# Performance work log

Measured on AMD Instinct MI355X. Metric: run time of the kernel, lower is better.

The kernel has to match this reference:

```python
import jax, jax.numpy as jnp
import numpy as np

N_NODES = 50000


def gcn_conv(x, edge_index, edge_weight, W, b):
    """PyG GCNConv: h = x @ W.T; symmetric-norm aggregate with self loops; + bias."""
    n = x.shape[0]
    row, col = edge_index[0], edge_index[1]
    loop = jnp.arange(n)
    row_f = jnp.concatenate([row, loop])
    col_f = jnp.concatenate([col, loop])
    ew_f = jnp.concatenate([edge_weight, jnp.ones((n,), dtype=edge_weight.dtype)])
    # degree at destination (col), D^{-1/2} A D^{-1/2}
    deg = jax.ops.segment_sum(ew_f, col_f, num_segments=n)
    dinv = jnp.where(deg > 0, jax.lax.rsqrt(deg), 0.0)
    norm = dinv[row_f] * ew_f * dinv[col_f]  # [E+N]
    h = x @ W.T  # [N, out]
    msg = h[row_f] * norm[:, None]  # [E+N, out]
    out = jax.ops.segment_sum(msg, col_f, num_segments=n)
    return out + b


def prelu(x, alpha):
    return jnp.where(x >= 0, x, alpha[None, :] * x)


def setup_inputs() -> dict:
    key = jax.random.key(0)
    ks = jax.random.split(key, 8)
    in_c, hid, hid2, E = 512, 128, 64, 800000
    x = jax.random.normal(ks[0], (N_NODES, in_c), dtype=jnp.float32)
    edge_index = jax.random.randint(ks[1], (2, E), 0, N_NODES, dtype=jnp.int64)
    edge_weight = jax.random.uniform(ks[2], (E,), dtype=jnp.float32)
    s1 = 1.0 / np.sqrt(in_c)
    s2 = 1.0 / np.sqrt(hid)
    W1 = jax.random.uniform(ks[3], (hid, in_c), minval=-s1, maxval=s1, dtype=jnp.float32)
    b1 = jnp.zeros((hid,), dtype=jnp.float32)
    alpha1 = jnp.full((hid,), 0.25, dtype=jnp.float32)
    W2 = jax.random.uniform(ks[4], (hid2, hid), minval=-s2, maxval=s2, dtype=jnp.float32)
    b2 = jnp.zeros((hid2,), dtype=jnp.float32)
    alpha2 = jnp.full((hid2,), 0.25, dtype=jnp.float32)
    return {"x": x, "edge_index": edge_index, "edge_weight": edge_weight,
            "W1": W1, "b1": b1, "alpha1": alpha1,
            "W2": W2, "b2": b2, "alpha2": alpha2}


def reference(x, edge_index, edge_weight, W1, b1, alpha1, W2, b2, alpha2):
    h = gcn_conv(x, edge_index, edge_weight, W1, b1)
    h = prelu(h, alpha1)
    h = gcn_conv(h, edge_index, edge_weight, W2, b2)
    h = prelu(h, alpha2)
    return h
```

## Files before the change

kernel.cpp:

```cpp
#include <hip/hip_runtime.h>
#include <hip/hip_fp16.h>

#define IN_C 512
#define HID  128
#define HID2 64
#define CPAD 32

typedef __attribute__((ext_vector_type(8))) short short8v;
typedef __attribute__((ext_vector_type(4))) float float4v;

__device__ __forceinline__ unsigned short f2bf(float f) {
  unsigned u = __float_as_uint(f);
  unsigned r = u + 0x7FFF + ((u >> 16) & 1);
  return (unsigned short)(r >> 16);
}
__device__ __forceinline__ float bf2f(unsigned short h) {
  return __uint_as_float((unsigned)h << 16);
}
__device__ __forceinline__ uint2 pack4(unsigned short a, unsigned short b,
                                       unsigned short c, unsigned short d) {
  uint2 p;
  p.x = (unsigned)a | ((unsigned)b << 16);
  p.y = (unsigned)c | ((unsigned)d << 16);
  return p;
}
__device__ __forceinline__ void split4(float4 v, uint2& hi, uint2& lo) {
  unsigned short h0 = f2bf(v.x), h1 = f2bf(v.y), h2 = f2bf(v.z), h3 = f2bf(v.w);
  unsigned short l0 = f2bf(v.x - bf2f(h0)), l1 = f2bf(v.y - bf2f(h1));
  unsigned short l2 = f2bf(v.z - bf2f(h2)), l3 = f2bf(v.w - bf2f(h3));
  hi = pack4(h0, h1, h2, h3);
  lo = pack4(l0, l1, l2, l3);
}

__global__ void k_detect(const unsigned* __restrict__ ei, int* __restrict__ flag) {
  __shared__ int nz;
  if (threadIdx.x == 0) nz = 0;
  __syncthreads();
  if (ei[2 * threadIdx.x + 1] != 0u) atomicOr(&nz, 1);
  __syncthreads();
  if (threadIdx.x == 0) *flag = (nz == 0) ? 1 : 0;
}

__device__ __forceinline__ int edge_at(const unsigned* __restrict__ ei, int f, int i) {
  return (int)(f ? ei[2 * (size_t)i] : ei[i]);
}

__global__ void k_wsplit(const float* __restrict__ W1, const float* __restrict__ W2,
                         short* __restrict__ w1h, short* __restrict__ w1l,
                         short* __restrict__ w2h, short* __restrict__ w2l) {
  int tid = blockIdx.x * blockDim.x + threadIdx.x;
  if (tid < 128 * (IN_C / 4)) {
    int n = tid >> 7, k = (tid & 127) * 4;
    float4 v = *(const float4*)(W1 + (size_t)n * IN_C + k);
    uint2 hi, lo;
    split4(v, hi, lo);
    size_t base = (((size_t)(k >> 3)) * 128 + n) * 8 + (k & 7);
    *(uint2*)(w1h + base) = hi;
    *(uint2*)(w1l + base) = lo;
  } else if (tid < 128 * (IN_C / 4) + 64 * (HID / 4)) {
    int t = tid - 128 * (IN_C / 4);
    int n = t >> 5, k = (t & 31) * 4;
    float4 v = *(const float4*)(W2 + (size_t)n * HID + k);
    uint2 hi, lo;
    split4(v, hi, lo);
    size_t base = (((size_t)(k >> 3)) * 64 + n) * 8 + (k & 7);
    *(uint2*)(w2h + base) = hi;
    *(uint2*)(w2l + base) = lo;
  }
}

__global__ void k_cnt(const unsigned* __restrict__ ei, const int* __restrict__ flag,
                      int* __restrict__ cntp, int* __restrict__ rank, int E) {
  int f = *flag;
  int stride = gridDim.x * blockDim.x * 2;
  for (int e = (blockIdx.x * blockDim.x + threadIdx.x) * 2; e < E; e += stride) {
    int c0, c1 = -1;
    if (f) {
      if (e + 1 < E) {
        uint4 v = *(const uint4*)(ei + 2 * (size_t)(E + e));
        c0 = (int)v.x;
        c1 = (int)v.z;
      } else {
        c0 = (int)ei[2 * (size_t)(E + e)];
      }
    } else {
      if (e + 1 < E) {
        uint2 v = *(const uint2*)(ei + (size_t)E + e);
        c0 = (int)v.x;
        c1 = (int)v.y;
      } else {
        c0 = (int)ei[(size_t)E + e];
      }
    }
    rank[e] = atomicAdd(&cntp[c0 * CPAD], 1);
    if (c1 >= 0) rank[e + 1] = atomicAdd(&cntp[c1 * CPAD], 1);
  }
}

__global__ __launch_bounds__(256) void k_scanA(const int* __restrict__ cntp,
                                               int* __restrict__ part,
                                               int* __restrict__ bsum, int N) {
  __shared__ int tmp[256];
  int t = threadIdx.x;
  int idx = blockIdx.x * 1024 + t * 4;
  int4 v;
  v.x = idx + 0 < N ? cntp[(size_t)(idx + 0) * CPAD] : 0;
  v.y = idx + 1 < N ? cntp[(size_t)(idx + 1) * CPAD] : 0;
  v.z = idx + 2 < N ? cntp[(size_t)(idx + 2) * CPAD] : 0;
  v.w = idx + 3 < N ? cntp[(size_t)(idx + 3) * CPAD] : 0;
  int s = v.x + v.y + v.z + v.w;
  tmp[t] = s;
  __syncthreads();
#pragma unroll
  for (int d = 1; d < 256; d <<= 1) {
    int u = (t >= d) ? tmp[t - d] : 0;
    __syncthreads();
    tmp[t] += u;
    __syncthreads();
  }
  int excl = tmp[t] - s;
  int4 o;
  o.x = excl;
  o.y = excl + v.x;
  o.z = excl + v.x + v.y;
  o.w = excl + v.x + v.y + v.z;
  if (idx + 3 < N) {
    *(int4*)(part + idx) = o;
  } else {
    if (idx + 0 < N) part[idx + 0] = o.x;
    if (idx + 1 < N) part[idx + 1] = o.y;
    if (idx + 2 < N) part[idx + 2] = o.z;
    if (idx + 3 < N) part[idx + 3] = o.w;
  }
  if (t == 255) bsum[blockIdx.x] = tmp[255];
}

__global__ __launch_bounds__(256) void k_scanB(int* __restrict__ bsum, int nb) {
  __shared__ int tmp[256];
  int t = threadIdx.x;
  int s = (t < nb) ? bsum[t] : 0;
  tmp[t] = s;
  __syncthreads();
#pragma unroll
  for (int d = 1; d < 256; d <<= 1) {
    int u = (t >= d) ? tmp[t - d] : 0;
    __syncthreads();
    tmp[t] += u;
    __syncthreads();
  }
  bsum[t] = tmp[t] - s;
}

__global__ void k_scanC(const int* __restrict__ part, const int* __restrict__ bsum,
                        int* __restrict__ rowptr, int N, int E) {
  int i = blockIdx.x * blockDim.x + threadIdx.x;
  if (i < N) rowptr[i] = part[i] + bsum[i >> 10];
  if (i == 0) rowptr[N] = E;
}

__global__ void k_fill(const unsigned* __restrict__ ei, const int* __restrict__ flag,
                       const float* __restrict__ ew, const int* __restrict__ rowptr,
                       const int* __restrict__ rank, uint2* __restrict__ ep, int E) {
  int f = *flag;
  int stride = gridDim.x * blockDim.x;
  for (int e = blockIdx.x * blockDim.x + threadIdx.x; e < E; e += stride) {
    int r = edge_at(ei, f, e);
    int c = edge_at(ei, f, E + e);
    int p = rowptr[c] + rank[e];
    uint2 m;
    m.x = (unsigned)r;
    m.y = __float_as_uint(ew[e]);
    ep[p] = m;
  }
}

__global__ void k_degsum(const uint2* __restrict__ ep, const int* __restrict__ rowptr,
                         float* __restrict__ dinv, int N) {
  int g = blockIdx.x * blockDim.x + threadIdx.x;
  int node = g >> 4, l = g & 15;
  if (node >= N) return;
  int s = rowptr[node], epd = rowptr[node + 1];
  float sum = 0.f;
  for (int p = s + l; p < epd; p += 16) sum += __uint_as_float(ep[p].y);
  sum += __shfl_xor(sum, 1);
  sum += __shfl_xor(sum, 2);
  sum += __shfl_xor(sum, 4);
  sum += __shfl_xor(sum, 8);
  if (l == 0) {
    float d = sum + 1.0f;
    float y = rsqrtf(d);
    y = y * (1.5f - 0.5f * d * y * y);
    dinv[node] = y;
  }
}

__global__ void k_scale(uint2* __restrict__ ep, const int* __restrict__ rowptr,
                        const float* __restrict__ dinv, int N) {
  int g = blockIdx.x * blockDim.x + threadIdx.x;
  int node = g >> 4, l = g & 15;
  if (node >= N) return;
  float dn = dinv[node];
  int s = rowptr[node], epd = rowptr[node + 1];
  for (int p = s + l; p < epd; p += 16) {
    uint2 m = ep[p];
    ep[p].y = __float_as_uint(dinv[m.x] * __uint_as_float(m.y) * dn);
  }
}

__global__ __launch_bounds__(256) void k_gemm1m(const float* __restrict__ x,
                                                const short* __restrict__ w1h,
                                                const short* __restrict__ w1l,
                                                __half* __restrict__ h, int M) {
  __shared__ short xh[4][128][8], xl[4][128][8];
  __shared__ short wh[4][128][8], wl[4][128][8];
  const int t = threadIdx.x;
  const int lane = t & 63, w = t >> 6;
  const int wm = (w >> 1) * 64, wn = (w & 1) * 64;
  const int kb = lane >> 4, r16 = lane & 15;
  const int m0 = blockIdx.x * 128;

  float4v acc[4][4];
#pragma unroll
  for (int mi = 0; mi < 4; mi++)
#pragma unroll
    for (int nj = 0; nj < 4; nj++) acc[mi][nj] = (float4v)0.f;

  for (int k0 = 0; k0 < IN_C; k0 += 32) {
#pragma unroll
    for (int i = 0; i < 4; i++) {
      int idx = t + i * 256;
      int row = idx >> 3, kc = idx & 7;
      int gr = m0 + row;
      if (gr >= M) gr = M - 1;
      float4 v = *(const float4*)(x + (size_t)gr * IN_C + k0 + kc * 4);
      uint2 hi, lo;
      split4(v, hi, lo);
      int kbw = kc >> 1, s = kc & 1;
      *(uint2*)&xh[kbw][row][s * 4] = hi;
      *(uint2*)&xl[kbw][row][s * 4] = lo;
    }
#pragma unroll
    for (int i = 0; i < 2; i++) {
      int idx = t + i * 256;
      int kb2 = idx >> 7, n = idx & 127;
      size_t gbase = (((size_t)(k0 >> 3) + kb2) * 128 + n) * 8;
      *(short8v*)&wh[kb2][n][0] = *(const short8v*)(w1h + gbase);
      *(short8v*)&wl[kb2][n][0] = *(const short8v*)(w1l + gbase);
    }
    __syncthreads();

    short8v ah[4], al[4], bh[4], bl[4];
#pragma unroll
    for (int mi = 0; mi < 4; mi++) {
      ah[mi] = *(short8v*)&xh[kb][wm + mi * 16 + r16][0];
      al[mi] = *(short8v*)&xl[kb][wm + mi * 16 + r16][0];
    }
#pragma unroll
    for (int nj = 0; nj < 4; nj++) {
      bh[nj] = *(short8v*)&wh[kb][wn + nj * 16 + r16][0];
      bl[nj] = *(short8v*)&wl[kb][wn + nj * 16 + r16][0];
    }
#pragma unroll
    for (int mi = 0; mi < 4; mi++)
#pragma unroll
      for (int nj = 0; nj < 4; nj++) {
        acc[mi][nj] = __builtin_amdgcn_mfma_f32_16x16x32_bf16(ah[mi], bh[nj], acc[mi][nj], 0, 0, 0);
        acc[mi][nj] = __builtin_amdgcn_mfma_f32_16x16x32_bf16(ah[mi], bl[nj], acc[mi][nj], 0, 0, 0);
        acc[mi][nj] = __builtin_amdgcn_mfma_f32_16x16x32_bf16(al[mi], bh[nj], acc[mi][nj], 0, 0, 0);
      }
    __syncthreads();
  }

#pragma unroll
  for (int mi = 0; mi < 4; mi++)
#pragma unroll
    for (int nj = 0; nj < 4; nj++) {
#pragma unroll
      for (int b = 0; b < 4; b++) {
        int grow = m0 + wm + mi * 16 + (lane >> 4) * 4 + b;
        int gcol = wn + nj * 16 + r16;
        if (grow < M) h[(size_t)grow * HID + gcol] = __float2half(acc[mi][nj][b]);
      }
    }
}

__global__ __launch_bounds__(256) void k_gemm2m(const float* __restrict__ z,
                                                const short* __restrict__ w2h,
                                                const short* __restrict__ w2l,
                                                __half* __restrict__ h, int M) {
  __shared__ short zh[4][128][8], zl[4][128][8];
  __shared__ short wh[4][64][8], wl[4][64][8];
  const int t = threadIdx.x;
  const int lane = t & 63, w = t >> 6;
  const int wm = (w >> 1) * 64, wn = (w & 1) * 32;
  const int kb = lane >> 4, r16 = lane & 15;
  const int m0 = blockIdx.x * 128;

  float4v acc[4][2];
#pragma unroll
  for (int mi = 0; mi < 4; mi++)
#pragma unroll
    for (int nj = 0; nj < 2; nj++) acc[mi][nj] = (float4v)0.f;

  for (int k0 = 0; k0 < HID; k0 += 32) {
#pragma unroll
    for (int i = 0; i < 4; i++) {
      int idx = t + i * 256;
      int row = idx >> 3, kc = idx & 7;
      int gr = m0 + row;
      if (gr >= M) gr = M - 1;
      float4 v = *(const float4*)(z + (size_t)gr * HID + k0 + kc * 4);
      uint2 hi, lo;
      split4(v, hi, lo);
      int kbw = kc >> 1, s = kc & 1;
      *(uint2*)&zh[kbw][row][s * 4] = hi;
      *(uint2*)&zl[kbw][row][s * 4] = lo;
    }
    {
      int kb2 = t >> 6, n = t & 63;
      size_t gbase = (((size_t)(k0 >> 3) + kb2) * 64 + n) * 8;
      *(short8v*)&wh[kb2][n][0] = *(const short8v*)(w2h + gbase);
      *(short8v*)&wl[kb2][n][0] = *(const short8v*)(w2l + gbase);
    }
    __syncthreads();

    short8v ah[4], al[4], bh[2], bl[2];
#pragma unroll
    for (int mi = 0; mi < 4; mi++) {
      ah[mi] = *(short8v*)&zh[kb][wm + mi * 16 + r16][0];
      al[mi] = *(short8v*)&zl[kb][wm + mi * 16 + r16][0];
    }
#pragma unroll
    for (int nj = 0; nj < 2; nj++) {
      bh[nj] = *(short8v*)&wh[kb][wn + nj * 16 + r16][0];
      bl[nj] = *(short8v*)&wl[kb][wn + nj * 16 + r16][0];
    }
#pragma unroll
    for (int mi = 0; mi < 4; mi++)
#pragma unroll
      for (int nj = 0; nj < 2; nj++) {
        acc[mi][nj] = __builtin_amdgcn_mfma_f32_16x16x32_bf16(ah[mi], bh[nj], acc[mi][nj], 0, 0, 0);
        acc[mi][nj] = __builtin_amdgcn_mfma_f32_16x16x32_bf16(ah[mi], bl[nj], acc[mi][nj], 0, 0, 0);
        acc[mi][nj] = __builtin_amdgcn_mfma_f32_16x16x32_bf16(al[mi], bh[nj], acc[mi][nj], 0, 0, 0);
      }
    __syncthreads();
  }

#pragma unroll
  for (int mi = 0; mi < 4; mi++)
#pragma unroll
    for (int nj = 0; nj < 2; nj++) {
#pragma unroll
      for (int b = 0; b < 4; b++) {
        int grow = m0 + wm + mi * 16 + (lane >> 4) * 4 + b;
        int gcol = wn + nj * 16 + r16;
        if (grow < M) h[(size_t)grow * HID2 + gcol] = __float2half(acc[mi][nj][b]);
      }
    }
}

__global__ void k_agg1(const __half* __restrict__ h, const int* __restrict__ rowptr,
                       const uint2* __restrict__ ep, const float* __restrict__ dinv,
                       const float* __restrict__ bias, const float* __restrict__ alpha,
                       float* __restrict__ z, int N) {
  int node = blockIdx.x * 4 + (threadIdx.x >> 6);
  int lane = threadIdx.x & 63;
  if (node >= N) return;
  const __half2* hp = (const __half2*)h;
  float2 acc = make_float2(0.f, 0.f);
  int s = rowptr[node];
  int dg = rowptr[node + 1] - s;
  for (int base = 0; base < dg; base += 64) {
    int k = base + lane;
    uint2 m = make_uint2(0u, 0u);
    if (k < dg) m = ep[s + k];
    int cnt = min(64, dg - base);
#pragma unroll 4
    for (int j = 0; j < cnt; j++) {
      int src = __shfl((int)m.x, j);
      float wv = __shfl(__uint_as_float(m.y), j);
      float2 v = __half22float2(hp[(size_t)src * 64 + lane]);
      acc.x += wv * v.x;
      acc.y += wv * v.y;
    }
  }
  float di = dinv[node];
  float sw = di * di;
  float2 v = __half22float2(hp[(size_t)node * 64 + lane]);
  acc.x += sw * v.x;
  acc.y += sw * v.y;
  acc.x += bias[lane * 2];
  acc.y += bias[lane * 2 + 1];
  float a0 = alpha[lane * 2], a1 = alpha[lane * 2 + 1];
  acc.x = acc.x >= 0.f ? acc.x : a0 * acc.x;
  acc.y = acc.y >= 0.f ? acc.y : a1 * acc.y;
  ((float2*)z)[(size_t)node * 64 + lane] = acc;
}

__global__ void k_agg2(const __half* __restrict__ h, const int* __restrict__ rowptr,
                       const uint2* __restrict__ ep, const float* __restrict__ dinv,
                       const float* __restrict__ bias, const float* __restrict__ alpha,
                       float* __restrict__ out, int N) {
  int node = blockIdx.x * 4 + (threadIdx.x >> 6);
  int lane = threadIdx.x & 63;
  if (node >= N) return;
  float acc = 0.f;
  int s = rowptr[node];
  int dg = rowptr[node + 1] - s;
  for (int base = 0; base < dg; base += 64) {
    int k = base + lane;
    uint2 m = make_uint2(0u, 0u);
    if (k < dg) m = ep[s + k];
    int cnt = min(64, dg - base);
#pragma unroll 4
    for (int j = 0; j < cnt; j++) {
      int src = __shfl((int)m.x, j);
      float wv = __shfl(__uint_as_float(m.y), j);
      acc += wv * __half2float(h[(size_t)src * HID2 + lane]);
    }
  }
  float di = dinv[node];
  acc += di * di * __half2float(h[(size_t)node * HID2 + lane]);
  acc += bias[lane];
  float a = alpha[lane];
  acc = acc >= 0.f ? acc : a * acc;
  out[(size_t)node * HID2 + lane] = acc;
}

extern "C" void kernel_launch(void* const* d_in, const int* in_sizes, int n_in,
                              void* d_out, int out_size, void* d_ws, size_t ws_size,
                              hipStream_t stream) {
  const float* x = (const float*)d_in[0];
  const unsigned* ei = (const unsigned*)d_in[1];
  const float* ew = (const float*)d_in[2];
  const float* W1 = (const float*)d_in[3];
  const float* b1 = (const float*)d_in[4];
  const float* a1 = (const float*)d_in[5];
  const float* W2 = (const float*)d_in[6];
  const float* b2 = (const float*)d_in[7];
  const float* a2 = (const float*)d_in[8];
  float* out = (float*)d_out;

  const int N = in_sizes[0] / IN_C;
  const int E = in_sizes[2];
  const int NB = (N + 1023) / 1024;

  char* w = (char*)d_ws;
  auto alloc = [&](size_t bytes) -> void* {
    void* p = (void*)w;
    w += (bytes + 255) / 256 * 256;
    return p;
  };
  int* flag = (int*)alloc(4);
  int* cntp = (int*)alloc((size_t)N * CPAD * 4);
  int* rank = (int*)alloc((size_t)E * 4);
  float* dinv = (float*)alloc((size_t)N * 4);
  int* rowptr = (int*)alloc((size_t)(N + 1) * 4);
  int* part = (int*)alloc((size_t)N * 4);
  int* bsum = (int*)alloc(256 * 4);
  uint2* ep = (uint2*)alloc((size_t)E * 8);
  short* w1h = (short*)alloc((size_t)HID * IN_C * 2);
  short* w1l = (short*)alloc((size_t)HID * IN_C * 2);
  short* w2h = (short*)alloc((size_t)HID2 * HID * 2);
  short* w2l = (short*)alloc((size_t)HID2 * HID * 2);
  __half* h1 = (__half*)alloc((size_t)N * HID * 2);
  float* z1 = (float*)alloc((size_t)N * HID * 4);
  __half* h2 = (__half*)alloc((size_t)N * HID2 * 2);

  hipMemsetAsync(cntp, 0, (size_t)N * CPAD * 4, stream);

  k_detect<<<1, 256, 0, stream>>>(ei, flag);
  k_wsplit<<<(128 * (IN_C / 4) + 64 * (HID / 4) + 255) / 256, 256, 0, stream>>>(
      W1, W2, w1h, w1l, w2h, w2l);
  k_cnt<<<1024, 256, 0, stream>>>(ei, flag, cntp, rank, E);
  k_scanA<<<NB, 256, 0, stream>>>(cntp, part, bsum, N);
  k_scanB<<<1, 256, 0, stream>>>(bsum, NB);
  k_scanC<<<(N + 255) / 256, 256, 0, stream>>>(part, bsum, rowptr, N, E);
  k_fill<<<1024, 256, 0, stream>>>(ei, flag, ew, rowptr, rank, ep, E);
  k_degsum<<<(N * 16 + 255) / 256, 256, 0, stream>>>(ep, rowptr, dinv, N);
  k_scale<<<(N * 16 + 255) / 256, 256, 0, stream>>>(ep, rowptr, dinv, N);

  k_gemm1m<<<(N + 127) / 128, 256, 0, stream>>>(x, w1h, w1l, h1, N);
  k_agg1<<<(N + 3) / 4, 256, 0, stream>>>(h1, rowptr, ep, dinv, b1, a1, z1, N);
  k_gemm2m<<<(N + 127) / 128, 256, 0, stream>>>(z1, w2h, w2l, h2, N);
  k_agg2<<<(N + 3) / 4, 256, 0, stream>>>(h2, rowptr, ep, dinv, b2, a2, out, N);
}
```

Measured before the change: 374.7 us.

## Drop LDS staging in GEMMs, load MFMA operands from global; fold scan pass

The two dense GEMMs stop staging x/z and the split weights through shared memory with barriers. Each wave now loads its A fragments directly from global memory into registers, splits them to bf16 hi/lo, and reads B fragments straight from the pre-split weight buffers, covering 64 rows and the full output width. The separate block-sum scan kernel is removed: scanC sums the preceding block totals in a loop for each element. This saves two barriers per k-step and one launch, in exchange for more register pressure (32 accumulators), repeated weight reads per wave through cache, and less coalesced global loads.

```diff
diff --git a/kernel.cpp b/kernel.cpp
--- a/kernel.cpp
+++ b/kernel.cpp
@@ -30,6 +30,15 @@
   unsigned short l2 = f2bf(v.z - bf2f(h2)), l3 = f2bf(v.w - bf2f(h3));
   hi = pack4(h0, h1, h2, h3);
   lo = pack4(l0, l1, l2, l3);
+}
+__device__ __forceinline__ void split8(float4 a, float4 b, short8v& hi, short8v& lo) {
+  uint2 h0, l0, h1, l1;
+  split4(a, h0, l0);
+  split4(b, h1, l1);
+  uint4 uh = make_uint4(h0.x, h0.y, h1.x, h1.y);
+  uint4 ul = make_uint4(l0.x, l0.y, l1.x, l1.y);
+  hi = *(short8v*)&uh;
+  lo = *(short8v*)&ul;
 }
 
 __global__ void k_detect(const unsigned* __restrict__ ei, int* __restrict__ flag) {
@@ -135,26 +144,15 @@
   if (t == 255) bsum[blockIdx.x] = tmp[255];
 }
 
-__global__ __launch_bounds__(256) void k_scanB(int* __restrict__ bsum, int nb) {
-  __shared__ int tmp[256];
-  int t = threadIdx.x;
-  int s = (t < nb) ? bsum[t] : 0;
-  tmp[t] = s;
-  __syncthreads();
-#pragma unroll
-  for (int d = 1; d < 256; d <<= 1) {
-    int u = (t >= d) ? tmp[t - d] : 0;
-    __syncthreads();
-    tmp[t] += u;
-    __syncthreads();
-  }
-  bsum[t] = tmp[t] - s;
-}
-
 __global__ void k_scanC(const int* __restrict__ part, const int* __restrict__ bsum,
-                        int* __restrict__ rowptr, int N, int E) {
+                        int* __restrict__ rowptr, int N, int E, int NB) {
   int i = blockIdx.x * blockDim.x + threadIdx.x;
-  if (i < N) rowptr[i] = part[i] + bsum[i >> 10];
+  if (i < N) {
+    int blk = i >> 10;
+    int off = 0;
+    for (int j = 0; j < blk; j++) off += bsum[j];
+    rowptr[i] = part[i] + off;
+  }
   if (i == 0) rowptr[N] = E;
 }
 
@@ -207,153 +205,115 @@
   }
 }
 
-__global__ __launch_bounds__(256) void k_gemm1m(const float* __restrict__ x,
+__global__ __launch_bounds__(256) void k_gemm1n(const float* __restrict__ x,
                                                 const short* __restrict__ w1h,
                                                 const short* __restrict__ w1l,
                                                 __half* __restrict__ h, int M) {
-  __shared__ short xh[4][128][8], xl[4][128][8];
-  __shared__ short wh[4][128][8], wl[4][128][8];
-  const int t = threadIdx.x;
-  const int lane = t & 63, w = t >> 6;
-  const int wm = (w >> 1) * 64, wn = (w & 1) * 64;
-  const int kb = lane >> 4, r16 = lane & 15;
-  const int m0 = blockIdx.x * 128;
-
-  float4v acc[4][4];
+  const int lane = threadIdx.x & 63, w = threadIdx.x >> 6;
+  const int row0 = blockIdx.x * 256 + w * 64;
+  const int kq = lane >> 4, r16 = lane & 15;
+
+  const float* px[4];
+#pragma unroll
+  for (int mi = 0; mi < 4; mi++) {
+    int gr = row0 + mi * 16 + r16;
+    if (gr >= M) gr = M - 1;
+    px[mi] = x + (size_t)gr * IN_C + kq * 8;
+  }
+
+  float4v acc[4][8];
 #pragma unroll
   for (int mi = 0; mi < 4; mi++)
 #pragma unroll
-    for (int nj = 0; nj < 4; nj++) acc[mi][nj] = (float4v)0.f;
+    for (int nj = 0; nj < 8; nj++) acc[mi][nj] = (float4v)0.f;
 
   for (int k0 = 0; k0 < IN_C; k0 += 32) {
-#pragma unroll
-    for (int i = 0; i < 4; i++) {
-      int idx = t + i * 256;
-      int row = idx >> 3, kc = idx & 7;
-      int gr = m0 + row;
-      if (gr >= M) gr = M - 1;
-      float4 v = *(const float4*)(x + (size_t)gr * IN_C + k0 + kc * 4);
-      uint2 hi, lo;
-      split4(v, hi, lo);
-      int kbw = kc >> 1, s = kc & 1;
-      *(uint2*)&xh[kbw][row][s * 4] = hi;
-      *(uint2*)&xl[kbw][row][s * 4] = lo;
-    }
-#pragma unroll
-    for (int i = 0; i < 2; i++) {
-      int idx = t + i * 256;
-      int kb2 = idx >> 7, n = idx & 127;
-      size_t gbase = (((size_t)(k0 >> 3) + kb2) * 128 + n) * 8;
-      *(short8v*)&wh[kb2][n][0] = *(const short8v*)(w1h + gbase);
-      *(short8v*)&wl[kb2][n][0] = *(const short8v*)(w1l + gbase);
-    }
-    __syncthreads();
-
-    short8v ah[4], al[4], bh[4], bl[4];
+    short8v ah[4], al[4];
 #pragma unroll
     for (int mi = 0; mi < 4; mi++) {
-      ah[mi] = *(short8v*)&xh[kb][wm + mi * 16 + r16][0];
-      al[mi] = *(short8v*)&xl[kb][wm + mi * 16 + r16][0];
-    }
-#pragma unroll
-    for (int nj = 0; nj < 4; nj++) {
-      bh[nj] = *(short8v*)&wh[kb][wn + nj * 16 + r16][0];
-      bl[nj] = *(short8v*)&wl[kb][wn + nj * 16 + r16][0];
-    }
-#pragma unroll
-    for (int mi = 0; mi < 4; mi++)
-#pragma unroll
-      for (int nj = 0; nj < 4; nj++) {
-        acc[mi][nj] = __builtin_amdgcn_mfma_f32_16x16x32_bf16(ah[mi], bh[nj], acc[mi][nj], 0, 0, 0);
-        acc[mi][nj] = __builtin_amdgcn_mfma_f32_16x16x32_bf16(ah[mi], bl[nj], acc[mi][nj], 0, 0, 0);
-        acc[mi][nj] = __builtin_amdgcn_mfma_f32_16x16x32_bf16(al[mi], bh[nj], acc[mi][nj], 0, 0, 0);
-      }
-    __syncthreads();
+      float4 a = *(const float4*)(px[mi] + k0);
+      float4 b = *(const float4*)(px[mi] + k0 + 4);
+      split8(a, b, ah[mi], al[mi]);
+    }
+#pragma unroll
+    for (int nj = 0; nj < 8; nj++) {
+      size_t gb = (((size_t)(k0 >> 3) + kq) * 128 + nj * 16 + r16) * 8;
+      short8v bh = *(const short8v*)(w1h + gb);
+      short8v bl = *(const short8v*)(w1l + gb);
+#pragma unroll
+      for (int mi = 0; mi < 4; mi++) {
+        acc[mi][nj] = __builtin_amdgcn_mfma_f32_16x16x32_bf16(ah[mi], bh, acc[mi][nj], 0, 0, 0);
+        acc[mi][nj] = __builtin_amdgcn_mfma_f32_16x16x32_bf16(ah[mi], bl, acc[mi][nj], 0, 0, 0);
+        acc[mi][nj] = __builtin_amdgcn_mfma_f32_16x16x32_bf16(al[mi], bh, acc[mi][nj], 0, 0, 0);
+      }
+    }
   }
 
 #pragma unroll
   for (int mi = 0; mi < 4; mi++)
 #pragma unroll
-    for (int nj = 0; nj < 4; nj++) {
+    for (int nj = 0; nj < 8; nj++) {
 #pragma unroll
       for (int b = 0; b < 4; b++) {
-        int grow = m0 + wm + mi * 16 + (lane >> 4) * 4 + b;
-        int gcol = wn + nj * 16 + r16;
+        int grow = row0 + mi * 16 + (lane >> 4) * 4 + b;
+        int gcol = nj * 16 + r16;
         if (grow < M) h[(size_t)grow * HID + gcol] = __float2half(acc[mi][nj][b]);
       }
     }
 }
 
-__global__ __launch_bounds__(256) void k_gemm2m(const float* __restrict__ z,
+__global__ __launch_bounds__(256) void k_gemm2n(const float* __restrict__ z,
                                                 const short* __restrict__ w2h,
                                                 const short* __restrict__ w2l,
                                                 __half* __restrict__ h, int M) {
-  __shared__ short zh[4][128][8], zl[4][128][8];
-  __shared__ short wh[4][64][8], wl[4][64][8];
-  const int t = threadIdx.x;
-  const int lane = t & 63, w = t >> 6;
-  const int wm = (w >> 1) * 64, wn = (w & 1) * 32;
-  const int kb = lane >> 4, r16 = lane & 15;
-  const int m0 = blockIdx.x * 128;
-
-  float4v acc[4][2];
+  const int lane = threadIdx.x & 63, w = threadIdx.x >> 6;
+  const int row0 = blockIdx.x * 256 + w * 64;
+  const int kq = lane >> 4, r16 = lane & 15;
+
+  const float* pz[4];
+#pragma unroll
+  for (int mi = 0; mi < 4; mi++) {
+    int gr = row0 + mi * 16 + r16;
+    if (gr >= M) gr = M - 1;
+    pz[mi] = z + (size_t)gr * HID + kq * 8;
+  }
+
+  float4v acc[4][4];
 #pragma unroll
   for (int mi = 0; mi < 4; mi++)
 #pragma unroll
-    for (int nj = 0; nj < 2; nj++) acc[mi][nj] = (float4v)0.f;
+    for (int nj = 0; nj < 4; nj++) acc[mi][nj] = (float4v)0.f;
 
   for (int k0 = 0; k0 < HID; k0 += 32) {
-#pragma unroll
-    for (int i = 0; i < 4; i++) {
-      int idx = t + i * 256;
-      int row = idx >> 3, kc = idx & 7;
-      int gr = m0 + row;
-      if (gr >= M) gr = M - 1;
-      float4 v = *(const float4*)(z + (size_t)gr * HID + k0 + kc * 4);
-      uint2 hi, lo;
-      split4(v, hi, lo);
-      int kbw = kc >> 1, s = kc & 1;
-      *(uint2*)&zh[kbw][row][s * 4] = hi;
-      *(uint2*)&zl[kbw][row][s * 4] = lo;
-    }
-    {
-      int kb2 = t >> 6, n = t & 63;
-      size_t gbase = (((size_t)(k0 >> 3) + kb2) * 64 + n) * 8;
-      *(short8v*)&wh[kb2][n][0] = *(const short8v*)(w2h + gbase);
-      *(short8v*)&wl[kb2][n][0] = *(const short8v*)(w2l + gbase);
-    }
-    __syncthreads();
-
-    short8v ah[4], al[4], bh[2], bl[2];
+    short8v ah[4], al[4];
 #pragma unroll
     for (int mi = 0; mi < 4; mi++) {
-      ah[mi] = *(short8v*)&zh[kb][wm + mi * 16 + r16][0];
-      al[mi] = *(short8v*)&zl[kb][wm + mi * 16 + r16][0];
-    }
-#pragma unroll
-    for (int nj = 0; nj < 2; nj++) {
-      bh[nj] = *(short8v*)&wh[kb][wn + nj * 16 + r16][0];
-      bl[nj] = *(short8v*)&wl[kb][wn + nj * 16 + r16][0];
-    }
-#pragma unroll
-    for (int mi = 0; mi < 4; mi++)
-#pragma unroll
-      for (int nj = 0; nj < 2; nj++) {
-        acc[mi][nj] = __builtin_amdgcn_mfma_f32_16x16x32_bf16(ah[mi], bh[nj], acc[mi][nj], 0, 0, 0);
-        acc[mi][nj] = __builtin_amdgcn_mfma_f32_16x16x32_bf16(ah[mi], bl[nj], acc[mi][nj], 0, 0, 0);
-        acc[mi][nj] = __builtin_amdgcn_mfma_f32_16x16x32_bf16(al[mi], bh[nj], acc[mi][nj], 0, 0, 0);
-      }
-    __syncthreads();
+      float4 a = *(const float4*)(pz[mi] + k0);
+      float4 b = *(const float4*)(pz[mi] + k0 + 4);
+      split8(a, b, ah[mi], al[mi]);
+    }
+#pragma unroll
+    for (int nj = 0; nj < 4; nj++) {
+      size_t gb = (((size_t)(k0 >> 3) + kq) * 64 + nj * 16 + r16) * 8;
+      short8v bh = *(const short8v*)(w2h + gb);
+      short8v bl = *(const short8v*)(w2l + gb);
+#pragma unroll
+      for (int mi = 0; mi < 4; mi++) {
+        acc[mi][nj] = __builtin_amdgcn_mfma_f32_16x16x32_bf16(ah[mi], bh, acc[mi][nj], 0, 0, 0);
+        acc[mi][nj] = __builtin_amdgcn_mfma_f32_16x16x32_bf16(ah[mi], bl, acc[mi][nj], 0, 0, 0);
+        acc[mi][nj] = __builtin_amdgcn_mfma_f32_16x16x32_bf16(al[mi], bh, acc[mi][nj], 0, 0, 0);
+      }
+    }
   }
 
 #pragma unroll
   for (int mi = 0; mi < 4; mi++)
 #pragma unroll
-    for (int nj = 0; nj < 2; nj++) {
+    for (int nj = 0; nj < 4; nj++) {
 #pragma unroll
       for (int b = 0; b < 4; b++) {
-        int grow = m0 + wm + mi * 16 + (lane >> 4) * 4 + b;
-        int gcol = wn + nj * 16 + r16;
+        int grow = row0 + mi * 16 + (lane >> 4) * 4 + b;
+        int gcol = nj * 16 + r16;
         if (grow < M) h[(size_t)grow * HID2 + gcol] = __float2half(acc[mi][nj][b]);
       }
     }
@@ -474,14 +434,13 @@
       W1, W2, w1h, w1l, w2h, w2l);
   k_cnt<<<1024, 256, 0, stream>>>(ei, flag, cntp, rank, E);
   k_scanA<<<NB, 256, 0, stream>>>(cntp, part, bsum, N);
-  k_scanB<<<1, 256, 0, stream>>>(bsum, NB);
-  k_scanC<<<(N + 255) / 256, 256, 0, stream>>>(part, bsum, rowptr, N, E);
+  k_scanC<<<(N + 255) / 256, 256, 0, stream>>>(part, bsum, rowptr, N, E, NB);
   k_fill<<<1024, 256, 0, stream>>>(ei, flag, ew, rowptr, rank, ep, E);
   k_degsum<<<(N * 16 + 255) / 256, 256, 0, stream>>>(ep, rowptr, dinv, N);
   k_scale<<<(N * 16 + 255) / 256, 256, 0, stream>>>(ep, rowptr, dinv, N);
 
-  k_gemm1m<<<(N + 127) / 128, 256, 0, stream>>>(x, w1h, w1l, h1, N);
+  k_gemm1n<<<(N + 255) / 256, 256, 0, stream>>>(x, w1h, w1l, h1, N);
   k_agg1<<<(N + 3) / 4, 256, 0, stream>>>(h1, rowptr, ep, dinv, b1, a1, z1, N);
-  k_gemm2m<<<(N + 127) / 128, 256, 0, stream>>>(z1, w2h, w2l, h2, N);
+  k_gemm2n<<<(N + 255) / 256, 256, 0, stream>>>(z1, w2h, w2l, h2, N);
   k_agg2<<<(N + 3) / 4, 256, 0, stream>>>(h2, rowptr, ep, dinv, b2, a2, out, N);
 }
```

After: 419.3 us. +11.9%, slower.
